# Performance work log

Hardware: AMD Instinct MI355X
Metric: run time of the kernel (lower is better)

The kernel has to match this reference:

```python
import jax, jax.numpy as jnp
import numpy as np

B, C, H, W = 128, 256, 32, 32
TD, NHEADS, PH, PW = 192, 4, 4, 4
FF = 384
MAXG = 8
TABLE = (2 * MAXG - 1) ** 2  # 225


def setup_inputs() -> dict:
    key = jax.random.key(0)
    ks = jax.random.split(key, 10)
    rn = lambda k, shape, s=0.02: jax.random.normal(k, shape, jnp.float32) * s
    return {
        "x": jax.random.normal(ks[0], (B, C, H, W), jnp.float32),
        "conv1_w": rn(ks[1], (TD, C)),          # 1x1 conv, no bias
        "conv2_w": rn(ks[2], (C, TD)),          # 1x1 conv, no bias
        "qkv_w": rn(ks[3], (TD, 3 * TD)), "qkv_b": jnp.zeros((3 * TD,), jnp.float32),
        "proj_w": rn(ks[4], (TD, TD)), "proj_b": jnp.zeros((TD,), jnp.float32),
        "ffn_w1": rn(ks[5], (TD, FF)), "ffn_b1": jnp.zeros((FF,), jnp.float32),
        "ffn_w2": rn(ks[6], (FF, TD)), "ffn_b2": jnp.zeros((TD,), jnp.float32),
        "ln1_g": jnp.ones((TD,), jnp.float32), "ln1_b": jnp.zeros((TD,), jnp.float32),
        "ln2_g": jnp.ones((TD,), jnp.float32), "ln2_b": jnp.zeros((TD,), jnp.float32),
        "alpha": rn(ks[7], (1,), 0.1),
        "rpb_table": rn(ks[8], (TABLE, NHEADS)),
    }


def _ln(x, g, b, eps=1e-5):
    m = x.mean(-1, keepdims=True)
    v = ((x - m) ** 2).mean(-1, keepdims=True)
    return (x - m) * jax.lax.rsqrt(v + eps) * g + b


def _rpb_index(Nh, Nw, maxg):
    # static (trace-time) relative position index over the patch grid
    ch, cw = np.meshgrid(np.arange(Nh), np.arange(Nw), indexing="ij")
    coords = np.stack([ch.ravel(), cw.ravel()])                 # (2, N)
    rel = coords[:, :, None] - coords[:, None, :]               # (2, N, N)
    idx = (rel[0] + maxg - 1) * (2 * maxg - 1) + (rel[1] + maxg - 1)
    return jnp.asarray(idx.reshape(-1), jnp.int32)              # (N*N,)


def reference(x, conv1_w, conv2_w, qkv_w, qkv_b, proj_w, proj_b,
              ffn_w1, ffn_b1, ffn_w2, ffn_b2,
              ln1_g, ln1_b, ln2_g, ln2_b, alpha, rpb_table):
    Nh, Nw = H // PH, W // PW
    Np = Nh * Nw
    hd = TD // NHEADS
    scale = 1.0 / np.sqrt(hd).astype(np.float32)

    # local 1x1 conv
    xl = jnp.einsum("bchw,tc->bthw", x, conv1_w)                # (B, TD, H, W)
    # patchify + mean-pool -> one token per patch
    xp = xl.reshape(B, TD, Nh, PH, Nw, PW).transpose(0, 2, 4, 3, 5, 1)
    xp = xp.reshape(B, Np, PH * PW, TD)
    tokens = xp.mean(axis=2)                                    # (B, Np, TD)

    # attention with gathered relative position bias
    t = _ln(tokens, ln1_g, ln1_b)
    qkv = (t @ qkv_w + qkv_b).reshape(B, Np, 3, NHEADS, hd)
    q, k, v = qkv[:, :, 0], qkv[:, :, 1], qkv[:, :, 2]          # (B, Np, H, hd)
    attn = jnp.einsum("bnhd,bmhd->bhnm", q, k) * scale
    bias = rpb_table[_rpb_index(Nh, Nw, MAXG)]                  # (Np*Np, heads)
    bias = bias.reshape(Np, Np, NHEADS).transpose(2, 0, 1)      # (heads, Np, Np)
    attn = jax.nn.softmax(attn + bias[None], axis=-1)
    o = jnp.einsum("bhnm,bmhd->bnhd", attn, v).reshape(B, Np, TD)
    o = o @ proj_w + proj_b

    out = tokens + alpha * o                                    # scaled residual
    h2 = _ln(out, ln2_g, ln2_b)
    out = out + (jax.nn.gelu(h2 @ ffn_w1 + ffn_b1, approximate=False) @ ffn_w2 + ffn_b2)

    # unpatchify: broadcast each token back over its ph*pw pixels
    ot = jnp.broadcast_to(out[:, :, None, :], (B, Np, PH * PW, TD))
    ot = ot.reshape(B, Nh, Nw, PH, PW, TD).transpose(0, 5, 1, 3, 2, 4)
    ot = ot.reshape(B, TD, H, W)
    return x + jnp.einsum("bthw,ct->bchw", ot, conv2_w)
```

## Files before the change

kernel.cpp:

```cpp
#include <hip/hip_runtime.h>
#include <hip/hip_bf16.h>

#define Bsz 128
#define Cch 256
#define Him 32
#define Wim 32
#define TD 192
#define NH 4
#define HD 48
#define FF 384
#define NP 64

typedef float f32x4 __attribute__((ext_vector_type(4)));
typedef __bf16 bf16x8 __attribute__((ext_vector_type(8)));
typedef unsigned int u32;

#define MFMA(a, b, c) __builtin_amdgcn_mfma_f32_16x16x32_bf16(a, b, c, 0, 0, 0)
#define LD8(p) (*reinterpret_cast<const bf16x8*>(p))
#define WAITV asm volatile("s_waitcnt vmcnt(0)" ::: "memory")

__device__ __forceinline__ ushort f2bf(float f) {
    union { __hip_bfloat16 h; ushort u; } cv;
    cv.h = __float2bfloat16(f);
    return cv.u;
}

__device__ __forceinline__ void gload16(const void* g, void* l) {
    __builtin_amdgcn_global_load_lds((const __attribute__((address_space(1))) u32*)g,
                                     (__attribute__((address_space(3))) u32*)l, 16, 0, 0);
}

template <int K2B>
__device__ __forceinline__ void stageW(char* lbuf, const char* g0, int colStrB, int tid) {
    constexpr int CHB = 32 * K2B;
    constexpr int NR = (CHB + 8191) / 8192;
#pragma unroll
    for (int rd = 0; rd < NR; ++rd) {
        int p = rd * 8192 + tid * 16;
        if (p < CHB) {
            int col = p / K2B;
            int kb = (p - col * K2B) ^ ((col & 7) << 4);
            gload16(g0 + (size_t)col * colStrB + kb, lbuf + p);
        }
    }
}

__global__ __launch_bounds__(256) void wprep_kernel(const float* __restrict__ c1,
                                                    const float* __restrict__ c2,
                                                    const float* __restrict__ qw,
                                                    const float* __restrict__ pw,
                                                    const float* __restrict__ f1,
                                                    const float* __restrict__ f2,
                                                    ushort* __restrict__ wb) {
    int g = blockIdx.x * 256 + threadIdx.x;
    float v;
    if (g < 49152) v = c1[g];
    else if (g < 98304) v = c2[g - 49152];
    else if (g < 208896) { int i = g - 98304;  int n = i / 192, k = i - n * 192; v = qw[k * 576 + n]; }
    else if (g < 245760) { int i = g - 208896; int n = i / 192, k = i - n * 192; v = pw[k * 192 + n]; }
    else if (g < 319488) { int i = g - 245760; int n = i / 192, k = i - n * 192; v = f1[k * 384 + n]; }
    else                 { int i = g - 319488; int n = i / 384, k = i - n * 384; v = f2[k * 192 + n]; }
    wb[g] = f2bf(v);
}

__global__ __launch_bounds__(256) void patchmean_kernel(const float* __restrict__ x,
                                                        ushort* __restrict__ xm) {
    int g = blockIdx.x * 256 + threadIdx.x;
    int nw = g & 7, nh = (g >> 3) & 7, c = (g >> 6) & 255, b = g >> 14;
    const float* px = x + ((size_t)(b * Cch + c) * Him + nh * 4) * Wim + nw * 4;
    float4 s0 = *reinterpret_cast<const float4*>(px);
    float4 s1 = *reinterpret_cast<const float4*>(px + Wim);
    float4 s2 = *reinterpret_cast<const float4*>(px + 2 * Wim);
    float4 s3 = *reinterpret_cast<const float4*>(px + 3 * Wim);
    float s = s0.x + s0.y + s0.z + s0.w + s1.x + s1.y + s1.z + s1.w +
              s2.x + s2.y + s2.z + s2.w + s3.x + s3.y + s3.z + s3.w;
    xm[(size_t)(b * NP + nh * 8 + nw) * Cch + c] = f2bf(s * 0.0625f);
}

__global__ __launch_bounds__(512, 2) void token_kernel(
    const ushort* __restrict__ xm, const ushort* __restrict__ wb,
    const float* __restrict__ qkv_b, const float* __restrict__ proj_b,
    const float* __restrict__ ffn_b1, const float* __restrict__ ffn_b2,
    const float* __restrict__ ln1_g, const float* __restrict__ ln1_b,
    const float* __restrict__ ln2_g, const float* __restrict__ ln2_b,
    const float* __restrict__ alphap, const float* __restrict__ rpb,
    float* __restrict__ y) {
    __shared__ __align__(16) char LDS[130048];
    ushort* tln = (ushort*)(LDS);
    ushort* qb  = (ushort*)(LDS + 25600);
    ushort* kb  = (ushort*)(LDS + 51200);
    ushort* vT  = (ushort*)(LDS + 76800);
    char*   SBB = LDS + 104448;
    float2* scr2 = (float2*)(LDS + 129024);
    ushort* t2  = tln;
    ushort* obp = qb;
    ushort* h0  = qb;
    ushort* h1  = kb;
    ushort* o2  = vT;
#define SBUF(i) (SBB + (i) * 12288)

    const int b = blockIdx.x;
    const int tid = threadIdx.x, lane = tid & 63, w = tid >> 6;
    const int l15 = lane & 15, slot = lane >> 4, slot16 = slot * 16;
    const int r = w >> 1, cc = w & 1;
    const int rowA = r * 16 + l15;
    const int orow = r * 16 + slot * 4;
    const int xp = (l15 & 7) << 4;
    const int colB = cc * 16 + l15;

    f32x4 tok[6];
    f32x4 pj[6];
#pragma unroll
    for (int c = 0; c < 6; ++c) { tok[c] = f32x4{0,0,0,0}; pj[c] = f32x4{0,0,0,0}; }

    {
        const char* xrow = (const char*)xm + ((size_t)(b * 64 + rowA)) * 512;
        bf16x8 a1[2][4];
#pragma unroll
        for (int kh = 0; kh < 2; ++kh)
#pragma unroll
            for (int ks = 0; ks < 4; ++ks)
                a1[kh][ks] = LD8(xrow + kh * 256 + ks * 64 + slot16);
        const char* c1g = (const char*)wb;
        stageW<256>(SBUF(0), c1g, 512, tid);
#pragma unroll
        for (int j = 0; j < 12; ++j) {
            WAITV; __syncthreads();
            if (j < 11) {
                int jn = j + 1;
                stageW<256>(SBUF(jn & 1), c1g + (size_t)(jn >> 1) * (32 * 512) + (jn & 1) * 256, 512, tid);
            }
            const char* bp = SBUF(j & 1) + colB * 256;
            int c = j >> 1, kh = j & 1;
#pragma unroll
            for (int ks = 0; ks < 4; ++ks) {
                int kbx = (ks * 64 + slot16) ^ xp;
                tok[c] = MFMA(a1[kh][ks], LD8(bp + kbx), tok[c]);
            }
        }
        stageW<384>(SBUF(0), (const char*)(wb + 98304), 384, tid);
        float s[4] = {}, s2[4] = {};
#pragma unroll
        for (int c = 0; c < 6; ++c)
#pragma unroll
            for (int j2 = 0; j2 < 4; ++j2) { float v = tok[c][j2]; s[j2] += v; s2[j2] += v * v; }
#pragma unroll
        for (int m = 1; m < 16; m <<= 1)
#pragma unroll
            for (int j2 = 0; j2 < 4; ++j2) { s[j2] += __shfl_xor(s[j2], m); s2[j2] += __shfl_xor(s2[j2], m); }
        if (l15 == 0)
#pragma unroll
            for (int j2 = 0; j2 < 4; ++j2) scr2[(orow + j2) * 2 + cc] = make_float2(s[j2], s2[j2]);
        __syncthreads();
#pragma unroll
        for (int j2 = 0; j2 < 4; ++j2) {
            int row = orow + j2;
            float2 eA = scr2[row * 2], eB = scr2[row * 2 + 1];
            float mean = (eA.x + eB.x) * (1.f / 192.f);
            float inv = rsqrtf((eA.y + eB.y) * (1.f / 192.f) - mean * mean + 1e-5f);
#pragma unroll
            for (int c = 0; c < 6; ++c) {
                int col = c * 32 + colB;
                tln[row * 200 + col] = f2bf((tok[c][j2] - mean) * inv * ln1_g[col] + ln1_b[col]);
            }
        }
    }

    {
        WAITV; __syncthreads();
        bf16x8 aT[6];
        const char* trow = (const char*)tln + rowA * 400;
#pragma unroll
        for (int ks = 0; ks < 6; ++ks) aT[ks] = LD8(trow + ks * 64 + slot16);
        const char* qg = (const char*)(wb + 98304);
#pragma unroll
        for (int j = 0; j < 18; ++j) {
            if (j) { WAITV; __syncthreads(); }
            if (j < 17) stageW<384>(SBUF((j + 1) & 1), qg + (size_t)(j + 1) * (32 * 384), 384, tid);
            const char* bp = SBUF(j & 1) + colB * 384;
            f32x4 acc = f32x4{0,0,0,0};
#pragma unroll
            for (int ks = 0; ks < 6; ++ks) {
                int kbx = (ks * 64 + slot16) ^ xp;
                acc = MFMA(aT[ks], LD8(bp + kbx), acc);
            }
            int col = (j % 6) * 32 + colB;
            if (j < 6) {
                float bias = qkv_b[col];
#pragma unroll
                for (int j2 = 0; j2 < 4; ++j2) qb[(orow + j2) * 200 + col] = f2bf(acc[j2] + bias);
            } else if (j < 12) {
                float bias = qkv_b[192 + col];
#pragma unroll
                for (int j2 = 0; j2 < 4; ++j2) kb[(orow + j2) * 200 + col] = f2bf(acc[j2] + bias);
            } else {
                float bias = qkv_b[384 + col];
                ushort4 pk;
                pk.x = f2bf(acc[0] + bias); pk.y = f2bf(acc[1] + bias);
                pk.z = f2bf(acc[2] + bias); pk.w = f2bf(acc[3] + bias);
                *reinterpret_cast<ushort4*>(&vT[col * 72 + orow]) = pk;
            }
        }
    }
    __syncthreads();

    {
        const float scale = 0.14433756729740643f;
        ushort* P2b0 = (ushort*)(LDS + cc * 9216);
        ushort* P2b1 = (ushort*)(LDS + 104448 + cc * 9216);
#pragma unroll
        for (int p = 0; p < 2; ++p) {
            int h = p * 2 + cc;
            ushort* P2 = p ? P2b1 : P2b0;
            float rb[4][4];
#pragma unroll
            for (int j2 = 0; j2 < 4; ++j2) {
                int qrow = orow + j2, qh = qrow >> 3, qw = qrow & 7;
#pragma unroll
                for (int nf = 0; nf < 4; ++nf) {
                    int krow = l15 + nf * 16;
                    rb[j2][nf] = rpb[((qh - (krow >> 3) + 7) * 15 + (qw - (krow & 7) + 7)) * 4 + h];
                }
            }
            uint4 z = make_uint4(0, 0, 0, 0);
            const char* qrp = (const char*)qb + rowA * 400 + h * 96;
            uint4 qa1 = *(const uint4*)(qrp + slot16);
            uint4 qa2 = (slot < 2) ? *(const uint4*)(qrp + 64 + slot16) : z;
            f32x4 S[4] = {};
#pragma unroll
            for (int nf = 0; nf < 4; ++nf) {
                const char* kp = (const char*)kb + (l15 + nf * 16) * 400 + h * 96;
                uint4 k1 = *(const uint4*)(kp + slot16);
                uint4 k2 = (slot < 2) ? *(const uint4*)(kp + 64 + slot16) : z;
                S[nf] = MFMA(*(bf16x8*)&qa1, *(bf16x8*)&k1, S[nf]);
                S[nf] = MFMA(*(bf16x8*)&qa2, *(bf16x8*)&k2, S[nf]);
            }
#pragma unroll
            for (int j2 = 0; j2 < 4; ++j2) {
                float sv[4]; float mx = -1e30f;
#pragma unroll
                for (int nf = 0; nf < 4; ++nf) { sv[nf] = S[nf][j2] * scale + rb[j2][nf]; mx = fmaxf(mx, sv[nf]); }
#pragma unroll
                for (int m = 1; m < 16; m <<= 1) mx = fmaxf(mx, __shfl_xor(mx, m));
                float sum = 0.f;
#pragma unroll
                for (int nf = 0; nf < 4; ++nf) { sv[nf] = expf(sv[nf] - mx); sum += sv[nf]; }
#pragma unroll
                for (int m = 1; m < 16; m <<= 1) sum += __shfl_xor(sum, m);
                float inv = 1.f / sum;
                int qrow = orow + j2;
#pragma unroll
                for (int nf = 0; nf < 4; ++nf) P2[qrow * 72 + l15 + nf * 16] = f2bf(sv[nf] * inv);
            }
        }
        __syncthreads();
#pragma unroll
        for (int p = 0; p < 2; ++p) {
            int h = p * 2 + cc;
            ushort* P2 = p ? P2b1 : P2b0;
            f32x4 O[3] = {};
            const char* prow = (const char*)P2 + rowA * 144;
#pragma unroll
            for (int ki = 0; ki < 2; ++ki) {
                bf16x8 pa = LD8(prow + ki * 64 + slot16);
#pragma unroll
                for (int nf = 0; nf < 3; ++nf) {
                    bf16x8 vb = LD8((const char*)vT + (h * 48 + l15 + nf * 16) * 144 + ki * 64 + slot16);
                    O[nf] = MFMA(pa, vb, O[nf]);
                }
            }
#pragma unroll
            for (int nf = 0; nf < 3; ++nf)
#pragma unroll
                for (int j2 = 0; j2 < 4; ++j2)
                    obp[(orow + j2) * 200 + h * 48 + l15 + nf * 16] = f2bf(O[nf][j2]);
        }
        __syncthreads();
        stageW<384>(SBUF(0), (const char*)(wb + 208896), 384, tid);
    }

    {
        WAITV; __syncthreads();
        bf16x8 aO[6];
        const char* orw = (const char*)obp + rowA * 400;
#pragma unroll
        for (int ks = 0; ks < 6; ++ks) aO[ks] = LD8(orw + ks * 64 + slot16);
        const char* pg = (const char*)(wb + 208896);
#pragma unroll
        for (int j = 0; j < 6; ++j) {
            if (j) { WAITV; __syncthreads(); }
            if (j < 5) stageW<384>(SBUF((j + 1) & 1), pg + (size_t)(j + 1) * (32 * 384), 384, tid);
            const char* bp = SBUF(j & 1) + colB * 384;
#pragma unroll
            for (int ks = 0; ks < 6; ++ks) {
                int kbx = (ks * 64 + slot16) ^ xp;
                pj[j] = MFMA(aO[ks], LD8(bp + kbx), pj[j]);
            }
        }
        stageW<384>(SBUF(0), (const char*)(wb + 245760), 384, tid);
        const float alpha = alphap[0];
        float s[4] = {}, s2[4] = {};
#pragma unroll
        for (int c = 0; c < 6; ++c) {
            int col = c * 32 + colB;
            float pb = proj_b[col];
#pragma unroll
            for (int j2 = 0; j2 < 4; ++j2) {
                float v = tok[c][j2] + alpha * (pj[c][j2] + pb);
                pj[c][j2] = v;
                s[j2] += v; s2[j2] += v * v;
            }
        }
#pragma unroll
        for (int m = 1; m < 16; m <<= 1)
#pragma unroll
            for (int j2 = 0; j2 < 4; ++j2) { s[j2] += __shfl_xor(s[j2], m); s2[j2] += __shfl_xor(s2[j2], m); }
        if (l15 == 0)
#pragma unroll
            for (int j2 = 0; j2 < 4; ++j2) scr2[(orow + j2) * 2 + cc] = make_float2(s[j2], s2[j2]);
        __syncthreads();
#pragma unroll
        for (int j2 = 0; j2 < 4; ++j2) {
            int row = orow + j2;
            float2 eA = scr2[row * 2], eB = scr2[row * 2 + 1];
            float mean = (eA.x + eB.x) * (1.f / 192.f);
            float inv = rsqrtf((eA.y + eB.y) * (1.f / 192.f) - mean * mean + 1e-5f);
#pragma unroll
            for (int c = 0; c < 6; ++c) {
                int col = c * 32 + colB;
                t2[row * 200 + col] = f2bf((pj[c][j2] - mean) * inv * ln2_g[col] + ln2_b[col]);
            }
        }
    }

    {
        WAITV; __syncthreads();
        bf16x8 aT2[6];
        const char* trow = (const char*)t2 + rowA * 400;
#pragma unroll
        for (int ks = 0; ks < 6; ++ks) aT2[ks] = LD8(trow + ks * 64 + slot16);
        const char* fg = (const char*)(wb + 245760);
#pragma unroll
        for (int j = 0; j < 12; ++j) {
            if (j) { WAITV; __syncthreads(); }
            if (j < 11) stageW<384>(SBUF((j + 1) & 1), fg + (size_t)(j + 1) * (32 * 384), 384, tid);
            const char* bp = SBUF(j & 1) + colB * 384;
            f32x4 acc = f32x4{0,0,0,0};
#pragma unroll
            for (int ks = 0; ks < 6; ++ks) {
                int kbx = (ks * 64 + slot16) ^ xp;
                acc = MFMA(aT2[ks], LD8(bp + kbx), acc);
            }
            int col384 = j * 32 + colB;
            float bias = ffn_b1[col384];
            ushort* hb = (j < 6) ? h0 : h1;
            int lcol = (j < 6) ? col384 : col384 - 192;
#pragma unroll
            for (int j2 = 0; j2 < 4; ++j2) {
                float v = acc[j2] + bias;
                v = 0.5f * v * (1.f + erff(v * 0.70710678118654752f));
                hb[(orow + j2) * 200 + lcol] = f2bf(v);
            }
        }
        stageW<384>(SBUF(0), (const char*)(wb + 319488), 768, tid);
    }

    {
        WAITV; __syncthreads();
        bf16x8 ah[2][6];
        const char* h0r = (const char*)h0 + rowA * 400;
        const char* h1r = (const char*)h1 + rowA * 400;
#pragma unroll
        for (int ks = 0; ks < 6; ++ks) {
            ah[0][ks] = LD8(h0r + ks * 64 + slot16);
            ah[1][ks] = LD8(h1r + ks * 64 + slot16);
        }
        const char* f2g = (const char*)(wb + 319488);
        f32x4 f2a[6];
#pragma unroll
        for (int c = 0; c < 6; ++c) f2a[c] = f32x4{0,0,0,0};
#pragma unroll
        for (int j = 0; j < 12; ++j) {
            if (j) { WAITV; __syncthreads(); }
            if (j < 11) {
                int jn = j + 1;
                stageW<384>(SBUF(jn & 1), f2g + (size_t)(jn >> 1) * (32 * 768) + (jn & 1) * 384, 768, tid);
            }
            const char* bp = SBUF(j & 1) + colB * 384;
            int c = j >> 1, kh = j & 1;
#pragma unroll
            for (int ks = 0; ks < 6; ++ks) {
                int kbx = (ks * 64 + slot16) ^ xp;
                f2a[c] = MFMA(ah[kh][ks], LD8(bp + kbx), f2a[c]);
            }
        }
        stageW<384>(SBUF(0), (const char*)(wb + 49152), 384, tid);
#pragma unroll
        for (int c = 0; c < 6; ++c) {
            int col = c * 32 + colB;
            float bias = ffn_b2[col];
#pragma unroll
            for (int j2 = 0; j2 < 4; ++j2)
                o2[(orow + j2) * 200 + col] = f2bf(pj[c][j2] + f2a[c][j2] + bias);
        }
    }

    {
        WAITV; __syncthreads();
        bf16x8 aO2[6];
        const char* o2r = (const char*)o2 + rowA * 400;
#pragma unroll
        for (int ks = 0; ks < 6; ++ks) aO2[ks] = LD8(o2r + ks * 64 + slot16);
        const char* c2g = (const char*)(wb + 49152);
        float* yb = y + (size_t)b * 64 * 256;
#pragma unroll
        for (int j = 0; j < 8; ++j) {
            if (j) { WAITV; __syncthreads(); }
            if (j < 7) stageW<384>(SBUF((j + 1) & 1), c2g + (size_t)(j + 1) * (32 * 384), 384, tid);
            const char* bp = SBUF(j & 1) + colB * 384;
            f32x4 acc = f32x4{0,0,0,0};
#pragma unroll
            for (int ks = 0; ks < 6; ++ks) {
                int kbx = (ks * 64 + slot16) ^ xp;
                acc = MFMA(aO2[ks], LD8(bp + kbx), acc);
            }
            int col = j * 32 + colB;
#pragma unroll
            for (int j2 = 0; j2 < 4; ++j2)
                yb[(size_t)(orow + j2) * 256 + col] = acc[j2];
        }
    }
#undef SBUF
}

__global__ __launch_bounds__(256) void final_kernel(const float* __restrict__ x,
                                                    const float* __restrict__ y,
                                                    float* __restrict__ out) {
    size_t g = (size_t)blockIdx.x * 256 + threadIdx.x;
    int w4 = g & 7, hh = (g >> 3) & 31, c = (g >> 8) & 255, b = (int)(g >> 16);
    int p = (hh >> 2) * 8 + w4;
    float yv = y[((size_t)b * NP + p) * Cch + c];
    float4 xv = reinterpret_cast<const float4*>(x)[g];
    reinterpret_cast<float4*>(out)[g] = make_float4(xv.x + yv, xv.y + yv, xv.z + yv, xv.w + yv);
}

extern "C" void kernel_launch(void* const* d_in, const int* in_sizes, int n_in,
                              void* d_out, int out_size, void* d_ws, size_t ws_size,
                              hipStream_t stream) {
    const float* x       = (const float*)d_in[0];
    const float* conv1_w = (const float*)d_in[1];
    const float* conv2_w = (const float*)d_in[2];
    const float* qkv_w   = (const float*)d_in[3];
    const float* qkv_b   = (const float*)d_in[4];
    const float* proj_w  = (const float*)d_in[5];
    const float* proj_b  = (const float*)d_in[6];
    const float* ffn_w1  = (const float*)d_in[7];
    const float* ffn_b1  = (const float*)d_in[8];
    const float* ffn_w2  = (const float*)d_in[9];
    const float* ffn_b2  = (const float*)d_in[10];
    const float* ln1_g   = (const float*)d_in[11];
    const float* ln1_b   = (const float*)d_in[12];
    const float* ln2_g   = (const float*)d_in[13];
    const float* ln2_b   = (const float*)d_in[14];
    const float* alpha   = (const float*)d_in[15];
    const float* rpb     = (const float*)d_in[16];
    float* out = (float*)d_out;

    float* ws_f = (float*)d_ws;
    float*  ybuf = ws_f;
    ushort* xm   = (ushort*)(ws_f + 2097152);
    ushort* wb   = xm + 2097152;

    wprep_kernel<<<1536, 256, 0, stream>>>(conv1_w, conv2_w, qkv_w, proj_w, ffn_w1, ffn_w2, wb);
    patchmean_kernel<<<8192, 256, 0, stream>>>(x, xm);
    token_kernel<<<Bsz, 512, 0, stream>>>(xm, wb, qkv_b, proj_b, ffn_b1, ffn_b2,
                                          ln1_g, ln1_b, ln2_g, ln2_b, alpha, rpb, ybuf);
    final_kernel<<<(Bsz * Cch * Him * Wim) / 1024, 256, 0, stream>>>(x, ybuf, out);
}
```

Before: 130.3 us.

## Deepen weight staging to 4-buffer pipeline, hoist biases, store y as bf16

Moves the token kernel's weight staging from double buffering to four buffers with three tiles in flight. Full vmcnt(0)+__syncthreads pairs are replaced by partial vmcnt waits plus raw s_barrier, and LDS grows to fit the extra buffers. Bias and LayerNorm parameters are hoisted into registers up front, and the intermediate y buffer is written as bf16 instead of fp32 to halve its traffic in final_kernel. The cost is lower occupancy (launch bounds changed to 1 block per CU, LDS near 150KB), more register pressure, and reduced precision in y.

Result: faster. 115.0 us (-11.7%).

```diff
diff --git a/kernel.cpp b/kernel.cpp
--- a/kernel.cpp
+++ b/kernel.cpp
@@ -17,7 +17,12 @@
 
 #define MFMA(a, b, c) __builtin_amdgcn_mfma_f32_16x16x32_bf16(a, b, c, 0, 0, 0)
 #define LD8(p) (*reinterpret_cast<const bf16x8*>(p))
-#define WAITV asm volatile("s_waitcnt vmcnt(0)" ::: "memory")
+#define VM0 asm volatile("s_waitcnt vmcnt(0)" ::: "memory")
+#define VM2 asm volatile("s_waitcnt vmcnt(2)" ::: "memory")
+#define VMB do { if (wlow) { asm volatile("s_waitcnt vmcnt(4)" ::: "memory"); } \
+                 else      { asm volatile("s_waitcnt vmcnt(2)" ::: "memory"); } } while (0)
+#define LGKM0 asm volatile("s_waitcnt lgkmcnt(0)" ::: "memory")
+#define SBAR __builtin_amdgcn_s_barrier()
 
 __device__ __forceinline__ ushort f2bf(float f) {
     union { __hip_bfloat16 h; ushort u; } cv;
@@ -77,21 +82,21 @@
     xm[(size_t)(b * NP + nh * 8 + nw) * Cch + c] = f2bf(s * 0.0625f);
 }
 
-__global__ __launch_bounds__(512, 2) void token_kernel(
+__global__ __launch_bounds__(512, 1) void token_kernel(
     const ushort* __restrict__ xm, const ushort* __restrict__ wb,
     const float* __restrict__ qkv_b, const float* __restrict__ proj_b,
     const float* __restrict__ ffn_b1, const float* __restrict__ ffn_b2,
     const float* __restrict__ ln1_g, const float* __restrict__ ln1_b,
     const float* __restrict__ ln2_g, const float* __restrict__ ln2_b,
     const float* __restrict__ alphap, const float* __restrict__ rpb,
-    float* __restrict__ y) {
-    __shared__ __align__(16) char LDS[130048];
+    ushort* __restrict__ y) {
+    __shared__ __align__(16) char LDS[154624];
     ushort* tln = (ushort*)(LDS);
     ushort* qb  = (ushort*)(LDS + 25600);
     ushort* kb  = (ushort*)(LDS + 51200);
     ushort* vT  = (ushort*)(LDS + 76800);
     char*   SBB = LDS + 104448;
-    float2* scr2 = (float2*)(LDS + 129024);
+    float2* scr2 = (float2*)(LDS + 153600);
     ushort* t2  = tln;
     ushort* obp = qb;
     ushort* h0  = qb;
@@ -107,38 +112,62 @@
     const int orow = r * 16 + slot * 4;
     const int xp = (l15 & 7) << 4;
     const int colB = cc * 16 + l15;
-
-    f32x4 tok[6];
-    f32x4 pj[6];
+    const bool wlow = (w < 4);
+
+    float qbr[18], f1br[12], l1gr[6], l1br[6], l2gr[6], l2br[6], pbr[6], f2br[6];
+#pragma unroll
+    for (int j = 0; j < 18; ++j) qbr[j] = qkv_b[(j / 6) * 192 + (j % 6) * 32 + colB];
+#pragma unroll
+    for (int j = 0; j < 12; ++j) f1br[j] = ffn_b1[j * 32 + colB];
+#pragma unroll
+    for (int c = 0; c < 6; ++c) {
+        int col = c * 32 + colB;
+        l1gr[c] = ln1_g[col]; l1br[c] = ln1_b[col];
+        l2gr[c] = ln2_g[col]; l2br[c] = ln2_b[col];
+        pbr[c] = proj_b[col]; f2br[c] = ffn_b2[col];
+    }
+    const float alpha = alphap[0];
+
+    const char* xrow = (const char*)xm + ((size_t)(b * 64 + rowA)) * 512;
+    bf16x8 a1[2][4];
+#pragma unroll
+    for (int kh = 0; kh < 2; ++kh)
+#pragma unroll
+        for (int ks = 0; ks < 4; ++ks)
+            a1[kh][ks] = LD8(xrow + kh * 256 + ks * 64 + slot16);
+
+    const char* c1g = (const char*)wb;
+    const char* qg  = (const char*)(wb + 98304);
+    const char* pg  = (const char*)(wb + 208896);
+    const char* fg  = (const char*)(wb + 245760);
+    const char* f2g = (const char*)(wb + 319488);
+    const char* c2g = (const char*)(wb + 49152);
+
+    f32x4 tok[6], pj[6];
 #pragma unroll
     for (int c = 0; c < 6; ++c) { tok[c] = f32x4{0,0,0,0}; pj[c] = f32x4{0,0,0,0}; }
 
-    {
-        const char* xrow = (const char*)xm + ((size_t)(b * 64 + rowA)) * 512;
-        bf16x8 a1[2][4];
-#pragma unroll
-        for (int kh = 0; kh < 2; ++kh)
-#pragma unroll
-            for (int ks = 0; ks < 4; ++ks)
-                a1[kh][ks] = LD8(xrow + kh * 256 + ks * 64 + slot16);
-        const char* c1g = (const char*)wb;
-        stageW<256>(SBUF(0), c1g, 512, tid);
-#pragma unroll
-        for (int j = 0; j < 12; ++j) {
-            WAITV; __syncthreads();
-            if (j < 11) {
-                int jn = j + 1;
-                stageW<256>(SBUF(jn & 1), c1g + (size_t)(jn >> 1) * (32 * 512) + (jn & 1) * 256, 512, tid);
-            }
-            const char* bp = SBUF(j & 1) + colB * 256;
-            int c = j >> 1, kh = j & 1;
-#pragma unroll
-            for (int ks = 0; ks < 4; ++ks) {
-                int kbx = (ks * 64 + slot16) ^ xp;
-                tok[c] = MFMA(a1[kh][ks], LD8(bp + kbx), tok[c]);
-            }
-        }
-        stageW<384>(SBUF(0), (const char*)(wb + 98304), 384, tid);
+    stageW<256>(SBUF(0), c1g, 512, tid);
+    stageW<256>(SBUF(1), c1g + 256, 512, tid);
+    stageW<256>(SBUF(2), c1g + 16384, 512, tid);
+#pragma unroll
+    for (int j = 0; j < 12; ++j) {
+        if (j < 10) VM2; else VM0;
+        SBAR;
+        if (j < 9) {
+            int jn = j + 3;
+            stageW<256>(SBUF(jn & 3), c1g + (size_t)(jn >> 1) * 16384 + (jn & 1) * 256, 512, tid);
+        }
+        const char* bp = SBUF(j & 3) + colB * 256;
+        int c = j >> 1, kh = j & 1;
+#pragma unroll
+        for (int ks = 0; ks < 4; ++ks)
+            tok[c] = MFMA(a1[kh][ks], LD8(bp + ((ks * 64 + slot16) ^ xp)), tok[c]);
+    }
+    stageW<384>(SBUF(0), qg, 384, tid);
+    stageW<384>(SBUF(1), qg + 12288, 384, tid);
+    stageW<384>(SBUF(2), qg + 24576, 384, tid);
+    {
         float s[4] = {}, s2[4] = {};
 #pragma unroll
         for (int c = 0; c < 6; ++c)
@@ -151,7 +180,7 @@
         if (l15 == 0)
 #pragma unroll
             for (int j2 = 0; j2 < 4; ++j2) scr2[(orow + j2) * 2 + cc] = make_float2(s[j2], s2[j2]);
-        __syncthreads();
+        LGKM0; SBAR;
 #pragma unroll
         for (int j2 = 0; j2 < 4; ++j2) {
             int row = orow + j2;
@@ -159,42 +188,36 @@
             float mean = (eA.x + eB.x) * (1.f / 192.f);
             float inv = rsqrtf((eA.y + eB.y) * (1.f / 192.f) - mean * mean + 1e-5f);
 #pragma unroll
-            for (int c = 0; c < 6; ++c) {
-                int col = c * 32 + colB;
-                tln[row * 200 + col] = f2bf((tok[c][j2] - mean) * inv * ln1_g[col] + ln1_b[col]);
-            }
-        }
-    }
-
-    {
-        WAITV; __syncthreads();
+            for (int c = 0; c < 6; ++c)
+                tln[row * 200 + c * 32 + colB] = f2bf((tok[c][j2] - mean) * inv * l1gr[c] + l1br[c]);
+        }
+        LGKM0; SBAR;
+    }
+
+    {
         bf16x8 aT[6];
         const char* trow = (const char*)tln + rowA * 400;
 #pragma unroll
         for (int ks = 0; ks < 6; ++ks) aT[ks] = LD8(trow + ks * 64 + slot16);
-        const char* qg = (const char*)(wb + 98304);
 #pragma unroll
         for (int j = 0; j < 18; ++j) {
-            if (j) { WAITV; __syncthreads(); }
-            if (j < 17) stageW<384>(SBUF((j + 1) & 1), qg + (size_t)(j + 1) * (32 * 384), 384, tid);
-            const char* bp = SBUF(j & 1) + colB * 384;
+            if (j < 16) VMB; else VM0;
+            SBAR;
+            if (j < 15) stageW<384>(SBUF((j + 3) & 3), qg + (size_t)(j + 3) * 12288, 384, tid);
+            const char* bp = SBUF(j & 3) + colB * 384;
             f32x4 acc = f32x4{0,0,0,0};
 #pragma unroll
-            for (int ks = 0; ks < 6; ++ks) {
-                int kbx = (ks * 64 + slot16) ^ xp;
-                acc = MFMA(aT[ks], LD8(bp + kbx), acc);
-            }
+            for (int ks = 0; ks < 6; ++ks)
+                acc = MFMA(aT[ks], LD8(bp + ((ks * 64 + slot16) ^ xp)), acc);
             int col = (j % 6) * 32 + colB;
+            float bias = qbr[j];
             if (j < 6) {
-                float bias = qkv_b[col];
 #pragma unroll
                 for (int j2 = 0; j2 < 4; ++j2) qb[(orow + j2) * 200 + col] = f2bf(acc[j2] + bias);
             } else if (j < 12) {
-                float bias = qkv_b[192 + col];
 #pragma unroll
                 for (int j2 = 0; j2 < 4; ++j2) kb[(orow + j2) * 200 + col] = f2bf(acc[j2] + bias);
             } else {
-                float bias = qkv_b[384 + col];
                 ushort4 pk;
                 pk.x = f2bf(acc[0] + bias); pk.y = f2bf(acc[1] + bias);
                 pk.z = f2bf(acc[2] + bias); pk.w = f2bf(acc[3] + bias);
@@ -202,7 +225,7 @@
             }
         }
     }
-    __syncthreads();
+    LGKM0; SBAR;
 
     {
         const float scale = 0.14433756729740643f;
@@ -253,7 +276,7 @@
                 for (int nf = 0; nf < 4; ++nf) P2[qrow * 72 + l15 + nf * 16] = f2bf(sv[nf] * inv);
             }
         }
-        __syncthreads();
+        LGKM0; SBAR;
 #pragma unroll
         for (int p = 0; p < 2; ++p) {
             int h = p * 2 + cc;
@@ -275,42 +298,42 @@
                 for (int j2 = 0; j2 < 4; ++j2)
                     obp[(orow + j2) * 200 + h * 48 + l15 + nf * 16] = f2bf(O[nf][j2]);
         }
-        __syncthreads();
-        stageW<384>(SBUF(0), (const char*)(wb + 208896), 384, tid);
-    }
-
-    {
-        WAITV; __syncthreads();
+        LGKM0; SBAR;
+    }
+    stageW<384>(SBUF(0), pg, 384, tid);
+    stageW<384>(SBUF(1), pg + 12288, 384, tid);
+    stageW<384>(SBUF(2), pg + 24576, 384, tid);
+
+    {
         bf16x8 aO[6];
         const char* orw = (const char*)obp + rowA * 400;
 #pragma unroll
         for (int ks = 0; ks < 6; ++ks) aO[ks] = LD8(orw + ks * 64 + slot16);
-        const char* pg = (const char*)(wb + 208896);
 #pragma unroll
         for (int j = 0; j < 6; ++j) {
-            if (j) { WAITV; __syncthreads(); }
-            if (j < 5) stageW<384>(SBUF((j + 1) & 1), pg + (size_t)(j + 1) * (32 * 384), 384, tid);
-            const char* bp = SBUF(j & 1) + colB * 384;
-#pragma unroll
-            for (int ks = 0; ks < 6; ++ks) {
-                int kbx = (ks * 64 + slot16) ^ xp;
-                pj[j] = MFMA(aO[ks], LD8(bp + kbx), pj[j]);
-            }
-        }
-        stageW<384>(SBUF(0), (const char*)(wb + 245760), 384, tid);
-        const float alpha = alphap[0];
+            if (j < 4) VMB; else VM0;
+            SBAR;
+            if (j < 3) stageW<384>(SBUF((j + 3) & 3), pg + (size_t)(j + 3) * 12288, 384, tid);
+            const char* bp = SBUF(j & 3) + colB * 384;
+#pragma unroll
+            for (int ks = 0; ks < 6; ++ks)
+                pj[j] = MFMA(aO[ks], LD8(bp + ((ks * 64 + slot16) ^ xp)), pj[j]);
+        }
+    }
+    SBAR;
+    stageW<384>(SBUF(0), fg, 384, tid);
+    stageW<384>(SBUF(1), fg + 12288, 384, tid);
+    stageW<384>(SBUF(2), fg + 24576, 384, tid);
+    {
         float s[4] = {}, s2[4] = {};
 #pragma unroll
-        for (int c = 0; c < 6; ++c) {
-            int col = c * 32 + colB;
-            float pb = proj_b[col];
+        for (int c = 0; c < 6; ++c)
 #pragma unroll
             for (int j2 = 0; j2 < 4; ++j2) {
-                float v = tok[c][j2] + alpha * (pj[c][j2] + pb);
+                float v = tok[c][j2] + alpha * (pj[c][j2] + pbr[c]);
                 pj[c][j2] = v;
                 s[j2] += v; s2[j2] += v * v;
             }
-        }
 #pragma unroll
         for (int m = 1; m < 16; m <<= 1)
 #pragma unroll
@@ -318,7 +341,7 @@
         if (l15 == 0)
 #pragma unroll
             for (int j2 = 0; j2 < 4; ++j2) scr2[(orow + j2) * 2 + cc] = make_float2(s[j2], s2[j2]);
-        __syncthreads();
+        LGKM0; SBAR;
 #pragma unroll
         for (int j2 = 0; j2 < 4; ++j2) {
             int row = orow + j2;
@@ -326,47 +349,47 @@
             float mean = (eA.x + eB.x) * (1.f / 192.f);
             float inv = rsqrtf((eA.y + eB.y) * (1.f / 192.f) - mean * mean + 1e-5f);
 #pragma unroll
-            for (int c = 0; c < 6; ++c) {
-                int col = c * 32 + colB;
-                t2[row * 200 + col] = f2bf((pj[c][j2] - mean) * inv * ln2_g[col] + ln2_b[col]);
-            }
-        }
-    }
-
-    {
-        WAITV; __syncthreads();
+            for (int c = 0; c < 6; ++c)
+                t2[row * 200 + c * 32 + colB] = f2bf((pj[c][j2] - mean) * inv * l2gr[c] + l2br[c]);
+        }
+        LGKM0; SBAR;
+    }
+
+    {
         bf16x8 aT2[6];
         const char* trow = (const char*)t2 + rowA * 400;
 #pragma unroll
         for (int ks = 0; ks < 6; ++ks) aT2[ks] = LD8(trow + ks * 64 + slot16);
-        const char* fg = (const char*)(wb + 245760);
 #pragma unroll
         for (int j = 0; j < 12; ++j) {
-            if (j) { WAITV; __syncthreads(); }
-            if (j < 11) stageW<384>(SBUF((j + 1) & 1), fg + (size_t)(j + 1) * (32 * 384), 384, tid);
-            const char* bp = SBUF(j & 1) + colB * 384;
+            if (j < 10) VMB; else VM0;
+            SBAR;
+            if (j < 9) stageW<384>(SBUF((j + 3) & 3), fg + (size_t)(j + 3) * 12288, 384, tid);
+            const char* bp = SBUF(j & 3) + colB * 384;
             f32x4 acc = f32x4{0,0,0,0};
 #pragma unroll
-            for (int ks = 0; ks < 6; ++ks) {
-                int kbx = (ks * 64 + slot16) ^ xp;
-                acc = MFMA(aT2[ks], LD8(bp + kbx), acc);
-            }
+            for (int ks = 0; ks < 6; ++ks)
+                acc = MFMA(aT2[ks], LD8(bp + ((ks * 64 + slot16) ^ xp)), acc);
             int col384 = j * 32 + colB;
-            float bias = ffn_b1[col384];
             ushort* hb = (j < 6) ? h0 : h1;
             int lcol = (j < 6) ? col384 : col384 - 192;
 #pragma unroll
             for (int j2 = 0; j2 < 4; ++j2) {
-                float v = acc[j2] + bias;
+                float v = acc[j2] + f1br[j];
                 v = 0.5f * v * (1.f + erff(v * 0.70710678118654752f));
                 hb[(orow + j2) * 200 + lcol] = f2bf(v);
             }
         }
-        stageW<384>(SBUF(0), (const char*)(wb + 319488), 768, tid);
-    }
-
-    {
-        WAITV; __syncthreads();
+    }
+    LGKM0; SBAR;
+    stageW<384>(SBUF(0), f2g, 768, tid);
+    stageW<384>(SBUF(1), f2g + 384, 768, tid);
+    stageW<384>(SBUF(2), f2g + 24576, 768, tid);
+
+    f32x4 f2a[6];
+#pragma unroll
+    for (int c = 0; c < 6; ++c) f2a[c] = f32x4{0,0,0,0};
+    {
         bf16x8 ah[2][6];
         const char* h0r = (const char*)h0 + rowA * 400;
         const char* h1r = (const char*)h1 + rowA * 400;
@@ -375,71 +398,67 @@
             ah[0][ks] = LD8(h0r + ks * 64 + slot16);
             ah[1][ks] = LD8(h1r + ks * 64 + slot16);
         }
-        const char* f2g = (const char*)(wb + 319488);
-        f32x4 f2a[6];
-#pragma unroll
-        for (int c = 0; c < 6; ++c) f2a[c] = f32x4{0,0,0,0};
 #pragma unroll
         for (int j = 0; j < 12; ++j) {
-            if (j) { WAITV; __syncthreads(); }
-            if (j < 11) {
-                int jn = j + 1;
-                stageW<384>(SBUF(jn & 1), f2g + (size_t)(jn >> 1) * (32 * 768) + (jn & 1) * 384, 768, tid);
-            }
-            const char* bp = SBUF(j & 1) + colB * 384;
+            if (j < 10) VMB; else VM0;
+            SBAR;
+            if (j < 9) {
+                int jn = j + 3;
+                stageW<384>(SBUF(jn & 3), f2g + (size_t)(jn >> 1) * 24576 + (jn & 1) * 384, 768, tid);
+            }
+            const char* bp = SBUF(j & 3) + colB * 384;
             int c = j >> 1, kh = j & 1;
 #pragma unroll
-            for (int ks = 0; ks < 6; ++ks) {
-                int kbx = (ks * 64 + slot16) ^ xp;
-                f2a[c] = MFMA(ah[kh][ks], LD8(bp + kbx), f2a[c]);
-            }
-        }
-        stageW<384>(SBUF(0), (const char*)(wb + 49152), 384, tid);
-#pragma unroll
-        for (int c = 0; c < 6; ++c) {
-            int col = c * 32 + colB;
-            float bias = ffn_b2[col];
-#pragma unroll
-            for (int j2 = 0; j2 < 4; ++j2)
-                o2[(orow + j2) * 200 + col] = f2bf(pj[c][j2] + f2a[c][j2] + bias);
-        }
-    }
-
-    {
-        WAITV; __syncthreads();
+            for (int ks = 0; ks < 6; ++ks)
+                f2a[c] = MFMA(ah[kh][ks], LD8(bp + ((ks * 64 + slot16) ^ xp)), f2a[c]);
+        }
+    }
+    stageW<384>(SBUF(0), c2g, 384, tid);
+    stageW<384>(SBUF(1), c2g + 12288, 384, tid);
+    stageW<384>(SBUF(2), c2g + 24576, 384, tid);
+#pragma unroll
+    for (int c = 0; c < 6; ++c) {
+        int col = c * 32 + colB;
+#pragma unroll
+        for (int j2 = 0; j2 < 4; ++j2)
+            o2[(orow + j2) * 200 + col] = f2bf(pj[c][j2] + f2a[c][j2] + f2br[c]);
+    }
+    LGKM0; SBAR;
+
+    {
         bf16x8 aO2[6];
         const char* o2r = (const char*)o2 + rowA * 400;
 #pragma unroll
         for (int ks = 0; ks < 6; ++ks) aO2[ks] = LD8(o2r + ks * 64 + slot16);
-        const char* c2g = (const char*)(wb + 49152);
-        float* yb = y + (size_t)b * 64 * 256;
+        ushort* yb = y + (size_t)b * 64 * 256;
 #pragma unroll
         for (int j = 0; j < 8; ++j) {
-            if (j) { WAITV; __syncthreads(); }
-            if (j < 7) stageW<384>(SBUF((j + 1) & 1), c2g + (size_t)(j + 1) * (32 * 384), 384, tid);
-            const char* bp = SBUF(j & 1) + colB * 384;
+            if (j < 6) VMB; else VM0;
+            SBAR;
+            if (j < 5) stageW<384>(SBUF((j + 3) & 3), c2g + (size_t)(j + 3) * 12288, 384, tid);
+            const char* bp = SBUF(j & 3) + colB * 384;
             f32x4 acc = f32x4{0,0,0,0};
 #pragma unroll
-            for (int ks = 0; ks < 6; ++ks) {
-                int kbx = (ks * 64 + slot16) ^ xp;
-                acc = MFMA(aO2[ks], LD8(bp + kbx), acc);
-            }
+            for (int ks = 0; ks < 6; ++ks)
+                acc = MFMA(aO2[ks], LD8(bp + ((ks * 64 + slot16) ^ xp)), acc);
             int col = j * 32 + colB;
 #pragma unroll
             for (int j2 = 0; j2 < 4; ++j2)
-                yb[(size_t)(orow + j2) * 256 + col] = acc[j2];
+                yb[(size_t)(orow + j2) * 256 + col] = f2bf(acc[j2]);
         }
     }
 #undef SBUF
 }
 
 __global__ __launch_bounds__(256) void final_kernel(const float* __restrict__ x,
-                                                    const float* __restrict__ y,
+                                                    const ushort* __restrict__ y,
                                                     float* __restrict__ out) {
     size_t g = (size_t)blockIdx.x * 256 + threadIdx.x;
     int w4 = g & 7, hh = (g >> 3) & 31, c = (g >> 8) & 255, b = (int)(g >> 16);
     int p = (hh >> 2) * 8 + w4;
-    float yv = y[((size_t)b * NP + p) * Cch + c];
+    u32 yu = y[((size_t)b * NP + p) * Cch + c];
+    union { u32 u; float f; } cv; cv.u = yu << 16;
+    float yv = cv.f;
     float4 xv = reinterpret_cast<const float4*>(x)[g];
     reinterpret_cast<float4*>(out)[g] = make_float4(xv.x + yv, xv.y + yv, xv.z + yv, xv.w + yv);
 }
@@ -466,9 +485,8 @@
     const float* rpb     = (const float*)d_in[16];
     float* out = (float*)d_out;
 
-    float* ws_f = (float*)d_ws;
-    float*  ybuf = ws_f;
-    ushort* xm   = (ushort*)(ws_f + 2097152);
+    ushort* ybuf = (ushort*)d_ws;
+    ushort* xm   = ybuf + 2097152;
     ushort* wb   = xm + 2097152;
 
     wprep_kernel<<<1536, 256, 0, stream>>>(conv1_w, conv2_w, qkv_w, proj_w, ffn_w1, ffn_w2, wb);
```
